# Kernel tuning notes

Measured on AMD Instinct MI355X. Metric: run time of the kernel, lower is better.

Reference implementation:

```python
import jax, jax.numpy as jnp
import numpy as np

SERIES_LEN = 4096
D_EMB = 1024
D_V = 1024
HURST = 0.7
H = HURST - 0.5          # exponent used by the module
DT = 1.0 / SERIES_LEN
EPS = 1e-8


def _attn_matrix():
    # Lower-triangular fractional power-law matrix A2[i, j]:
    #   j <  i : ((i - j) * dt + 1e-8) ** (hurst - 0.5)
    #   j == i : 1e-8 ** (hurst - 0.5)
    #   j >  i : 0
    i = jnp.arange(SERIES_LEN, dtype=jnp.int32)[:, None]
    j = jnp.arange(SERIES_LEN, dtype=jnp.int32)[None, :]
    diff = jnp.clip(i - j, 1, None).astype(jnp.float32)  # safe base for fractional power
    lower = jnp.where(i > j, (diff * DT + EPS) ** H, 0.0)
    diag = jnp.eye(SERIES_LEN, dtype=jnp.float32) * (EPS ** H)
    return lower + diag  # (L, L) float32


def setup_inputs() -> dict:
    key = jax.random.key(0)
    k1, k2 = jax.random.split(key)
    embed_series = jax.random.normal(k1, (D_EMB, SERIES_LEN), dtype=jnp.float32)
    # nn.Linear(d_emb, d_v, bias=False) weight has shape (d_v, d_emb)
    Wv_weight = jax.random.normal(k2, (D_V, D_EMB), dtype=jnp.float32) * (1.0 / np.sqrt(D_EMB))
    return {"embed_series": embed_series, "Wv_weight": Wv_weight}


def reference(embed_series, Wv_weight):
    # V (original, d_v x L) = Wv(embed_series.T).T ; output[i, c] = sum_j A2[i, j] * V[c, j]
    # => out = A2 @ (embed_series.T @ Wv_weight.T), shape (L, d_v)
    A2 = _attn_matrix()                                   # (L, L) lower triangular
    Y = jnp.einsum('el,ve->lv', embed_series, Wv_weight)  # (L, d_v)
    return A2 @ Y                                         # (L, d_v)
```

## Files before the change

kernel.cpp:

```cpp
#include <hip/hip_runtime.h>
#include <hip/hip_bf16.h>
#include <cstdint>
#include <cstddef>


#define L_SER 4096
#define DEMB  1024
#define DV    1024

#define R_STRIDE 4352
#define R_O0     4096

typedef __bf16 bf16_t;
typedef __attribute__((ext_vector_type(8))) __bf16 bf16x8;
typedef __attribute__((ext_vector_type(4))) float f32x4;

__device__ __forceinline__ void glds16(const bf16_t* g, bf16_t* l) {
    __builtin_amdgcn_global_load_lds(
        (const __attribute__((address_space(1))) unsigned int*)(const void*)g,
        (__attribute__((address_space(3))) unsigned int*)(void*)l,
        16, 0, 0);
}

__global__ void prep_kernel(const float* __restrict__ E, const float* __restrict__ W,
                            bf16_t* __restrict__ Eb, bf16_t* __restrict__ Wb,
                            bf16_t* __restrict__ R) {
    const int b = blockIdx.x;
    if (b < 136) {
        int idx = b * 256 + threadIdx.x;
        int s = idx / R_STRIDE;
        int x = idx - s * R_STRIDE;
        int d = R_O0 + s - x;
        float v = 0.0f;
        if (d >= 0 && d < L_SER)
            v = powf((d == 0) ? 1e-8f : ((float)d * (1.0f / (float)L_SER) + 1e-8f), 0.2f);
        R[idx] = (bf16_t)v;
    } else if (b < 136 + 2048) {
        int idx = (b - 136) * 256 + threadIdx.x;
        const f32x4* s = (const f32x4*)E;
        f32x4 v0 = s[idx * 2], v1 = s[idx * 2 + 1];
        bf16x8 o;
        o[0] = (bf16_t)v0[0]; o[1] = (bf16_t)v0[1]; o[2] = (bf16_t)v0[2]; o[3] = (bf16_t)v0[3];
        o[4] = (bf16_t)v1[0]; o[5] = (bf16_t)v1[1]; o[6] = (bf16_t)v1[2]; o[7] = (bf16_t)v1[3];
        ((bf16x8*)Eb)[idx] = o;
    } else {
        int idx = (b - 2184) * 256 + threadIdx.x;
        const f32x4* s = (const f32x4*)W;
        f32x4 v0 = s[idx * 2], v1 = s[idx * 2 + 1];
        bf16x8 o;
        o[0] = (bf16_t)v0[0]; o[1] = (bf16_t)v0[1]; o[2] = (bf16_t)v0[2]; o[3] = (bf16_t)v0[3];
        o[4] = (bf16_t)v1[0]; o[5] = (bf16_t)v1[1]; o[6] = (bf16_t)v1[2]; o[7] = (bf16_t)v1[3];
        ((bf16x8*)Wb)[idx] = o;
    }
}

#define GA_LANES()                                                           \
    const int tid  = threadIdx.x;                                            \
    const int wave = tid >> 6;                                               \
    const int lane = tid & 63;                                               \
    const int quad = lane >> 4;                                              \
    const int ln   = lane & 15;                                              \
    const int wm   = wave >> 1;                                              \
    const int wn   = wave & 1;                                               \
    const int lrow = lane >> 3;                                              \
    const int lch  = (lane & 7) ^ lrow;                                      \
    const int rsw   = ln & 7;                                                \
    const int coff0 = ((quad ^ rsw)) * 8;                                    \
    const int coff1 = (((4 + quad) ^ rsw)) * 8;

#define GA2_STAGE(SBOFS, WOFS)                                               \
    _Pragma("unroll")                                                        \
    for (int c = 0; c < 8; ++c) {                                            \
        glds16(pB[c], &sB[(SBOFS) + (c * 16 + wave * 4) * 128]);             \
        pB[c] += 128;                                                        \
    }                                                                        \
    glds16(pRwin, &sW[(WOFS) + wave * 512]);                                 \
    pRwin += 128;

#define GA2_COMPUTE(SBOFS, WOFS)                                             \
    _Pragma("unroll")                                                        \
    for (int kk = 0; kk < 4; ++kk) {                                         \
        const int co = (((kk * 4 + quad) ^ rsw)) * 8;                        \
        bf16x8 afr[4], bfr[4];                                               \
        _Pragma("unroll")                                                    \
        for (int tm = 0; tm < 4; ++tm)                                       \
            afr[tm] = *(const bf16x8*)&sW[(WOFS) + awbase + (kk * 32 + quad * 8 - 16 * tm)]; \
        _Pragma("unroll")                                                    \
        for (int tn = 0; tn < 4; ++tn)                                       \
            bfr[tn] = *(const bf16x8*)&sB[(SBOFS) + (wn * 64 + tn * 16 + ln) * 128 + co]; \
        _Pragma("unroll")                                                    \
        for (int tm = 0; tm < 4; ++tm)                                       \
            _Pragma("unroll")                                                \
            for (int tn = 0; tn < 4; ++tn)                                   \
                acc[tm][tn] = __builtin_amdgcn_mfma_f32_16x16x32_bf16(afr[tm], bfr[tn], acc[tm][tn], 0, 0, 0); \
    }

__global__ __launch_bounds__(256, 2) void gemm_a_kernel(const bf16_t* __restrict__ R,
                                                        const bf16_t* __restrict__ Eb,
                                                        bf16_t* __restrict__ T0,
                                                        bf16_t* __restrict__ T1) {
    __shared__ __align__(16) bf16_t sB[2 * 128 * 128];
    __shared__ __align__(16) bf16_t sW[2 * 2048];

    const int bid = blockIdx.x;
    int I, nb, h;
    if (bid < 256) { I = bid >> 3;                nb = bid & 7;         h = 0; }
    else           { I = 31 - ((bid - 256) >> 3); nb = (bid - 256) & 7; h = 1; }
    const int i0 = I * 128;
    const int n0 = nb * 128;
    const int c0 = h ? ((I + 2) & ~1) : 0;
    const int nsteps2 = h ? ((2 * (I + 1) - c0) >> 1) : ((I + 2) >> 1);
    const int j0b = c0 * 64;
    bf16_t* __restrict__ Tout = h ? T1 : T0;

    GA_LANES()

    const int awbase = (ln & 7) * 248 + 120 - 64 * wm - 8 * (ln >> 3);

    f32x4 acc[4][4];
#pragma unroll
    for (int a = 0; a < 4; ++a)
#pragma unroll
        for (int b = 0; b < 4; ++b) acc[a][b] = (f32x4){0, 0, 0, 0};

    if (nsteps2 > 0) {
        int wrow = tid / 31;
        int wchk = tid - wrow * 31;
        if (tid >= 248) { wrow = 7; wchk = 30; }
        const bf16_t* pRwin = R + (size_t)wrow * R_STRIDE + (R_O0 - i0 + j0b - 120 + wchk * 8);

        const int r4  = lane >> 4;
        const int sch = (lane & 15) ^ (((wave & 1) * 4 + r4) & 7);
        const bf16_t* pB[8];
#pragma unroll
        for (int c = 0; c < 8; ++c)
            pB[c] = Eb + (size_t)(n0 + c * 16 + wave * 4 + r4) * L_SER + j0b + sch * 8;

        GA2_STAGE(0, 0)
        for (int s = 0;; s += 2) {
            __syncthreads();
            if (s + 1 < nsteps2) { GA2_STAGE(128 * 128, 2048) }
            GA2_COMPUTE(0, 0)
            if (s + 1 >= nsteps2) break;
            __syncthreads();
            if (s + 2 < nsteps2) { GA2_STAGE(0, 0) }
            GA2_COMPUTE(128 * 128, 2048)
            if (s + 2 >= nsteps2) break;
        }
    }

#pragma unroll
    for (int tm = 0; tm < 4; ++tm) {
        int row_base = i0 + wm * 64 + tm * 16 + quad * 4;
#pragma unroll
        for (int tn = 0; tn < 4; ++tn) {
            int col = n0 + wn * 64 + tn * 16 + ln;
#pragma unroll
            for (int r = 0; r < 4; ++r)
                Tout[(size_t)(row_base + r) * DEMB + col] = (bf16_t)acc[tm][tn][r];
        }
    }
}

#define GB_STAGE(SBOFS)                                                      \
    _Pragma("unroll")                                                        \
    for (int c = 0; c < 4; ++c) {                                            \
        glds16(pA[c], &sA[(SBOFS) + (c * 32 + wave * 8) * 64]);              \
        glds16(pW[c], &sBB[(SBOFS) + (c * 32 + wave * 8) * 64]);             \
        pA[c] += 64; pW[c] += 64;                                            \
    }

#define GB_COMPUTE(SBOFS)                                                    \
    _Pragma("unroll")                                                        \
    for (int kk = 0; kk < 2; ++kk) {                                         \
        const int co = kk ? coff1 : coff0;                                   \
        bf16x8 afr[4], bfr[4];                                               \
        _Pragma("unroll")                                                    \
        for (int c = 0; c < 4; ++c)                                          \
            afr[c] = *(const bf16x8*)&sA[(SBOFS) + (((c >> 1) * 64) + wm * 32 + (c & 1) * 16 + ln) * 64 + co]; \
        _Pragma("unroll")                                                    \
        for (int tn = 0; tn < 4; ++tn)                                       \
            bfr[tn] = *(const bf16x8*)&sBB[(SBOFS) + (wn * 64 + tn * 16 + ln) * 64 + co]; \
        _Pragma("unroll")                                                    \
        for (int t = 0; t < 2; ++t)                                          \
            _Pragma("unroll")                                                \
            for (int tn = 0; tn < 4; ++tn)                                   \
                acc[t][tn] = __builtin_amdgcn_mfma_f32_16x16x32_bf16(afr[t], bfr[tn], acc[t][tn], 0, 0, 0); \
        _Pragma("unroll")                                                    \
        for (int t = 0; t < 2; ++t)                                          \
            _Pragma("unroll")                                                \
            for (int tn = 0; tn < 4; ++tn)                                   \
                acc[t][tn] = __builtin_amdgcn_mfma_f32_16x16x32_bf16(afr[2 + t], bfr[tn], acc[t][tn], 0, 0, 0); \
    }

__global__ __launch_bounds__(256, 2) void gemm_b_kernel(const bf16_t* __restrict__ T0,
                                                        const bf16_t* __restrict__ T1,
                                                        const bf16_t* __restrict__ Wb,
                                                        float* __restrict__ out) {
    __shared__ __align__(16) bf16_t sA[2 * 128 * 64];
    __shared__ __align__(16) bf16_t sBB[2 * 128 * 64];

    const int bid = blockIdx.x;
    const int ib = bid >> 3;
    const int nb = bid & 7;
    const int i0 = ib * 64;
    const int n0 = nb * 128;

    GA_LANES()

    f32x4 acc[2][4];
#pragma unroll
    for (int a = 0; a < 2; ++a)
#pragma unroll
        for (int b = 0; b < 4; ++b) acc[a][b] = (f32x4){0, 0, 0, 0};

    const int nsteps = DEMB / 64;

    const bf16_t* pA[4];
    const bf16_t* pW[4];
#pragma unroll
    for (int c = 0; c < 4; ++c) {
        const bf16_t* base = (c < 2) ? T0 : T1;
        int rr = (c & 1) * 32 + wave * 8 + lrow;
        pA[c] = base + (size_t)(i0 + rr) * DEMB + lch * 8;
        pW[c] = Wb + (size_t)(n0 + c * 32 + wave * 8 + lrow) * DEMB + lch * 8;
    }

    GB_STAGE(0)
    for (int s = 0;; s += 2) {
        __syncthreads();
        if (s + 1 < nsteps) { GB_STAGE(128 * 64) }
        GB_COMPUTE(0)
        if (s + 1 >= nsteps) break;
        __syncthreads();
        if (s + 2 < nsteps) { GB_STAGE(0) }
        GB_COMPUTE(128 * 64)
        if (s + 2 >= nsteps) break;
    }

#pragma unroll
    for (int t = 0; t < 2; ++t) {
        int row_base = i0 + wm * 32 + t * 16 + quad * 4;
#pragma unroll
        for (int tn = 0; tn < 4; ++tn) {
            int col = n0 + wn * 64 + tn * 16 + ln;
#pragma unroll
            for (int r = 0; r < 4; ++r)
                out[(size_t)(row_base + r) * DV + col] = acc[t][tn][r];
        }
    }
}

extern "C" void kernel_launch(void* const* d_in, const int* in_sizes, int n_in,
                              void* d_out, int out_size, void* d_ws, size_t ws_size,
                              hipStream_t stream) {
    const float* E = (const float*)d_in[0];
    const float* W = (const float*)d_in[1];
    float* out = (float*)d_out;

    char* ws = (char*)d_ws;
    bf16_t* Eb = (bf16_t*)(ws);
    bf16_t* T0 = (bf16_t*)(ws + (size_t)8  * 1024 * 1024);
    bf16_t* T1 = (bf16_t*)(ws + (size_t)16 * 1024 * 1024);
    bf16_t* Wb = (bf16_t*)(ws + (size_t)24 * 1024 * 1024);
    bf16_t* R  = (bf16_t*)(ws + (size_t)26 * 1024 * 1024);

    prep_kernel<<<2696, 256, 0, stream>>>(E, W, Eb, Wb, R);
    gemm_a_kernel<<<512, 256, 0, stream>>>(R, Eb, T0, T1);
    gemm_b_kernel<<<512, 256, 0, stream>>>(T0, T1, Wb, out);
}
```

Measured before the change: 117.5 us.

## Load W operand directly to registers and widen K step with swizzled LDS

The second GEMM kernel now keeps only the A operand (T0/T1 rows) in LDS and loads the W operand straight from global memory into double-buffered register arrays. The K step doubles from 64 to 128, and A is staged with an XOR-swizzled column layout to avoid LDS bank conflicts. This removes the LDS traffic and space for W and halves the number of barriers. In exchange it uses many more VGPRs for the W buffers, which could cause spills or lower occupancy under launch_bounds(256,2), and the direct global loads of W are less coalesced.

```diff
diff --git a/kernel.cpp b/kernel.cpp
--- a/kernel.cpp
+++ b/kernel.cpp
@@ -162,43 +162,47 @@
     }
 }
 
-#define GB_STAGE(SBOFS)                                                      \
-    _Pragma("unroll")                                                        \
-    for (int c = 0; c < 4; ++c) {                                            \
-        glds16(pA[c], &sA[(SBOFS) + (c * 32 + wave * 8) * 64]);              \
-        glds16(pW[c], &sBB[(SBOFS) + (c * 32 + wave * 8) * 64]);             \
-        pA[c] += 64; pW[c] += 64;                                            \
-    }
-
-#define GB_COMPUTE(SBOFS)                                                    \
-    _Pragma("unroll")                                                        \
-    for (int kk = 0; kk < 2; ++kk) {                                         \
-        const int co = kk ? coff1 : coff0;                                   \
-        bf16x8 afr[4], bfr[4];                                               \
+#define GB2_STAGE_A(SBOFS)                                                   \
+    _Pragma("unroll")                                                        \
+    for (int c = 0; c < 8; ++c) {                                            \
+        glds16(pA[c], &sA[(SBOFS) + (c * 16 + wave * 4) * 128]);             \
+        pA[c] += 128;                                                        \
+    }
+
+#define GB2_WLOAD(WB)                                                        \
+    _Pragma("unroll")                                                        \
+    for (int kk = 0; kk < 4; ++kk)                                           \
+        _Pragma("unroll")                                                    \
+        for (int tn = 0; tn < 4; ++tn)                                       \
+            WB[kk * 4 + tn] = *(const bf16x8*)(pW[tn] + kk * 32 + quad * 8); \
+    _Pragma("unroll")                                                        \
+    for (int tn = 0; tn < 4; ++tn) pW[tn] += 128;
+
+#define GB2_COMPUTE(SBOFS, WB)                                               \
+    _Pragma("unroll")                                                        \
+    for (int kk = 0; kk < 4; ++kk) {                                         \
+        const int co = (((kk * 4 + quad) ^ rsw)) * 8;                        \
+        bf16x8 afr[4];                                                       \
         _Pragma("unroll")                                                    \
         for (int c = 0; c < 4; ++c)                                          \
-            afr[c] = *(const bf16x8*)&sA[(SBOFS) + (((c >> 1) * 64) + wm * 32 + (c & 1) * 16 + ln) * 64 + co]; \
-        _Pragma("unroll")                                                    \
-        for (int tn = 0; tn < 4; ++tn)                                       \
-            bfr[tn] = *(const bf16x8*)&sBB[(SBOFS) + (wn * 64 + tn * 16 + ln) * 64 + co]; \
+            afr[c] = *(const bf16x8*)&sA[(SBOFS) + (((c >> 1) * 64) + wm * 32 + (c & 1) * 16 + ln) * 128 + co]; \
         _Pragma("unroll")                                                    \
         for (int t = 0; t < 2; ++t)                                          \
             _Pragma("unroll")                                                \
             for (int tn = 0; tn < 4; ++tn)                                   \
-                acc[t][tn] = __builtin_amdgcn_mfma_f32_16x16x32_bf16(afr[t], bfr[tn], acc[t][tn], 0, 0, 0); \
+                acc[t][tn] = __builtin_amdgcn_mfma_f32_16x16x32_bf16(afr[t], WB[kk * 4 + tn], acc[t][tn], 0, 0, 0); \
         _Pragma("unroll")                                                    \
         for (int t = 0; t < 2; ++t)                                          \
             _Pragma("unroll")                                                \
             for (int tn = 0; tn < 4; ++tn)                                   \
-                acc[t][tn] = __builtin_amdgcn_mfma_f32_16x16x32_bf16(afr[2 + t], bfr[tn], acc[t][tn], 0, 0, 0); \
+                acc[t][tn] = __builtin_amdgcn_mfma_f32_16x16x32_bf16(afr[2 + t], WB[kk * 4 + tn], acc[t][tn], 0, 0, 0); \
     }
 
 __global__ __launch_bounds__(256, 2) void gemm_b_kernel(const bf16_t* __restrict__ T0,
                                                         const bf16_t* __restrict__ T1,
                                                         const bf16_t* __restrict__ Wb,
                                                         float* __restrict__ out) {
-    __shared__ __align__(16) bf16_t sA[2 * 128 * 64];
-    __shared__ __align__(16) bf16_t sBB[2 * 128 * 64];
+    __shared__ __align__(16) bf16_t sA[2 * 128 * 128];
 
     const int bid = blockIdx.x;
     const int ib = bid >> 3;
@@ -214,27 +218,34 @@
 #pragma unroll
         for (int b = 0; b < 4; ++b) acc[a][b] = (f32x4){0, 0, 0, 0};
 
-    const int nsteps = DEMB / 64;
-
-    const bf16_t* pA[4];
+    const int nsteps = DEMB / 128;
+
+    const int r4  = lane >> 4;
+    const int sch = (lane & 15) ^ (((wave & 1) * 4 + r4) & 7);
+    const bf16_t* pA[8];
+#pragma unroll
+    for (int c = 0; c < 8; ++c) {
+        const bf16_t* base = (c < 4) ? T0 : T1;
+        int rr = (c & 3) * 16 + wave * 4 + r4;
+        pA[c] = base + (size_t)(i0 + rr) * DEMB + sch * 8;
+    }
     const bf16_t* pW[4];
 #pragma unroll
-    for (int c = 0; c < 4; ++c) {
-        const bf16_t* base = (c < 2) ? T0 : T1;
-        int rr = (c & 1) * 32 + wave * 8 + lrow;
-        pA[c] = base + (size_t)(i0 + rr) * DEMB + lch * 8;
-        pW[c] = Wb + (size_t)(n0 + c * 32 + wave * 8 + lrow) * DEMB + lch * 8;
-    }
-
-    GB_STAGE(0)
+    for (int tn = 0; tn < 4; ++tn)
+        pW[tn] = Wb + (size_t)(n0 + wn * 64 + tn * 16 + ln) * DEMB;
+
+    bf16x8 wb0[16], wb1[16];
+
+    GB2_WLOAD(wb0)
+    GB2_STAGE_A(0)
     for (int s = 0;; s += 2) {
         __syncthreads();
-        if (s + 1 < nsteps) { GB_STAGE(128 * 64) }
-        GB_COMPUTE(0)
+        if (s + 1 < nsteps) { GB2_STAGE_A(128 * 128) GB2_WLOAD(wb1) }
+        GB2_COMPUTE(0, wb0)
         if (s + 1 >= nsteps) break;
         __syncthreads();
-        if (s + 2 < nsteps) { GB_STAGE(0) }
-        GB_COMPUTE(128 * 64)
+        if (s + 2 < nsteps) { GB2_STAGE_A(0) GB2_WLOAD(wb0) }
+        GB2_COMPUTE(128 * 128, wb1)
         if (s + 2 >= nsteps) break;
     }
 
```

New measurement: 134.8 us. 1.15x slower.
